# Kernel optimization log

Hardware: AMD Instinct MI355X
Metric: run time of the kernel (lower is better)

## Reference

```python
import jax, jax.numpy as jnp
import numpy as np

M, K, N = 8192, 1024, 8192

def setup_inputs() -> dict:
    key = jax.random.key(0)
    k1, k2, k3, k4 = jax.random.split(key, 4)
    # a, b are int8-valued quantized tensors (stored as int32 per harness dtype set)
    a = jax.random.randint(k1, (M, K), 0, 127, dtype=jnp.int32)
    b = jax.random.randint(k2, (K, N), 0, 127, dtype=jnp.int32)
    alpha_row = jax.random.uniform(k3, (M, 1), dtype=jnp.float32)
    alpha_col = jax.random.uniform(k4, (1, N), dtype=jnp.float32)
    return {"a": a, "b": b, "alpha_row": alpha_row, "alpha_col": alpha_col}

def reference(a, b, alpha_row, alpha_col):
    # Faithful to TorchGemmA8W8.forward: upcast int8 operands to fp32,
    # matmul with fp32 accumulate, cast result to int8.
    # (alpha_row / alpha_col are accepted but unused in this variant.)
    x = jnp.matmul(a.astype(jnp.float32), b.astype(jnp.float32))  # [M, N] fp32
    return x.astype(jnp.int8)
```

## Files before the change

### kernel.cpp

```cpp
#include <hip/hip_runtime.h>
#include <stdint.h>

#define M_DIM 8192
#define N_DIM 8192
#define K_DIM 1024
#define BK    128

typedef int int4v __attribute__((ext_vector_type(4)));

__device__ __forceinline__ void gload16(const char* g, char* l) {
    __builtin_amdgcn_global_load_lds(
        (__attribute__((address_space(1))) void*)(void*)const_cast<char*>(g),
        (__attribute__((address_space(3))) void*)l,
        16, 0, 0);
}

__device__ __forceinline__ int sat8(int v) {
    v = v > 127 ? 127 : v;
    v = v < -128 ? -128 : v;
    return v;
}

__global__ __launch_bounds__(256) void pack_ab_kernel(const int* __restrict__ a,
                                                      const int* __restrict__ b,
                                                      int* __restrict__ outA,
                                                      char* __restrict__ outB) {
    __shared__ char tile[64][68];
    const int t = threadIdx.x;
    if (blockIdx.x < 8192) {
        int i = blockIdx.x * 256 + t;
        int4 v = ((const int4*)a)[i];
        outA[i] = (v.x & 0xff) | ((v.y & 0xff) << 8) |
                  ((v.z & 0xff) << 16) | ((v.w & 0xff) << 24);
        return;
    }
    const int bx = blockIdx.x - 8192;
    const int n0 = (bx & 127) * 64;
    const int k0 = (bx >> 7) * 64;
    const int tr  = t >> 4;
    const int tc4 = (t & 15) << 2;
#pragma unroll
    for (int j = 0; j < 4; ++j) {
        int row = tr + j * 16;
        int4 v = *(const int4*)&b[(size_t)(k0 + row) * N_DIM + n0 + tc4];
        tile[row][tc4 + 0] = (char)v.x;
        tile[row][tc4 + 1] = (char)v.y;
        tile[row][tc4 + 2] = (char)v.z;
        tile[row][tc4 + 3] = (char)v.w;
    }
    __syncthreads();
#pragma unroll
    for (int j = 0; j < 4; ++j) {
        int n = tr + j * 16;
        int pk = (tile[tc4 + 0][n] & 0xff) |
                 ((tile[tc4 + 1][n] & 0xff) << 8) |
                 ((tile[tc4 + 2][n] & 0xff) << 16) |
                 ((tile[tc4 + 3][n] & 0xff) << 24);
        *(int*)&outB[(size_t)(n0 + n) * K_DIM + k0 + tc4] = pk;
    }
}

__global__ __launch_bounds__(256) void gemm_i8_kernel(const char* __restrict__ A8,
                                                      const char* __restrict__ B8,
                                                      int* __restrict__ C) {
    __shared__ __align__(16) char As[2 * 128 * 64];
    __shared__ __align__(16) char Bs[2 * 128 * 64];

    const int t    = threadIdx.x;
    const int bn   = blockIdx.x;
    const int bm   = blockIdx.y;
    const int lane = t & 63;
    const int wave = t >> 6;
    const int wm   = wave >> 1;
    const int wn   = wave & 1;
    const int quad = lane >> 4;
    const int l16  = lane & 15;

    const size_t aBase = (size_t)(bm * 128) * K_DIM;
    const size_t bBase = (size_t)(bn * 128) * K_DIM;

    const int sr = t >> 2;
    const int swzc = (((t & 3) ^ ((t >> 3) & 3)) << 4);
    const int laneByte = ((quad ^ ((l16 >> 1) & 3)) << 4);

    int4v acc[4][4] = {};

    for (int kt = 0; kt < K_DIM / BK; ++kt) {
        const int kOff = kt * BK;
#pragma unroll
        for (int s = 0; s < 4; ++s) {
            const int p = s >> 1;
            const int rr = ((s & 1) << 6) + sr;
            const int f = s * 4096 + t * 16;
            gload16(A8 + aBase + (size_t)rr * K_DIM + kOff + p * 64 + swzc, As + f);
            gload16(B8 + bBase + (size_t)rr * K_DIM + kOff + p * 64 + swzc, Bs + f);
        }
        __syncthreads();

#pragma unroll
        for (int h = 0; h < 2; ++h) {
            int4v af[4], bf[4];
#pragma unroll
            for (int mi = 0; mi < 4; ++mi)
                af[mi] = *(const int4v*)
                    &As[h * 8192 + (wm * 64 + mi * 16 + l16) * 64 + laneByte];
#pragma unroll
            for (int ni = 0; ni < 4; ++ni)
                bf[ni] = *(const int4v*)
                    &Bs[h * 8192 + (wn * 64 + ni * 16 + l16) * 64 + laneByte];

#pragma unroll
            for (int mi = 0; mi < 4; ++mi)
#pragma unroll
                for (int ni = 0; ni < 4; ++ni)
                    acc[mi][ni] = __builtin_amdgcn_mfma_i32_16x16x64_i8(
                        af[mi], bf[ni], acc[mi][ni], 0, 0, 0);
        }

        __syncthreads();
    }

    const int mBase = bm * 128 + wm * 64;
    const int nBase = bn * 128 + wn * 64;
#pragma unroll
    for (int mi = 0; mi < 4; ++mi) {
#pragma unroll
        for (int ni = 0; ni < 4; ++ni) {
            const int col = nBase + ni * 16 + l16;
#pragma unroll
            for (int r = 0; r < 4; ++r) {
                const int row = mBase + mi * 16 + quad * 4 + r;
                C[(size_t)row * N_DIM + col] = sat8(acc[mi][ni][r]);
            }
        }
    }
}

__global__ __launch_bounds__(256) void gemm_naive_kernel(const int* __restrict__ a,
                                                         const int* __restrict__ b,
                                                         int* __restrict__ C) {
    const int col = blockIdx.x * 256 + threadIdx.x;
    const int row = blockIdx.y;
    int acc = 0;
    for (int k = 0; k < K_DIM; ++k)
        acc += a[(size_t)row * K_DIM + k] * b[(size_t)k * N_DIM + col];
    C[(size_t)row * N_DIM + col] = sat8(acc);
}

extern "C" void kernel_launch(void* const* d_in, const int* in_sizes, int n_in,
                              void* d_out, int out_size, void* d_ws, size_t ws_size,
                              hipStream_t stream) {
    const int* a = (const int*)d_in[0];
    const int* b = (const int*)d_in[1];
    int* out = (int*)d_out;

    const size_t needed = 2 * (size_t)M_DIM * K_DIM;
    if (ws_size < needed) {
        gemm_naive_kernel<<<dim3(N_DIM / 256, M_DIM), 256, 0, stream>>>(a, b, out);
        return;
    }

    char* A8 = (char*)d_ws;
    char* B8 = A8 + (size_t)M_DIM * K_DIM;

    pack_ab_kernel<<<8192 + 2048, 256, 0, stream>>>(a, b, (int*)A8, B8);
    gemm_i8_kernel<<<dim3(N_DIM / 128, M_DIM / 128), 256, 0, stream>>>(A8, B8, out);
}
```

Baseline: 363.3 us.

## Triple-buffer LDS tiles with async prefetch two K-steps ahead

Replaces the load-then-sync double-half loop with a three-slot LDS ring of BK=64 tiles. Global-to-LDS loads for tile kt+2 are issued before the MFMAs of tile kt, and a single barrier per iteration is gated by s_waitcnt vmcnt(4) instead of full syncthreads. MFMA sections are wrapped in s_setprio to favour compute issue. This aims to hide global memory latency behind compute, at the cost of more LDS use, which may reduce occupancy, and redundant loads of the last tile at the tail.

```diff
diff --git a/kernel.cpp b/kernel.cpp
--- a/kernel.cpp
+++ b/kernel.cpp
@@ -4,7 +4,6 @@
 #define M_DIM 8192
 #define N_DIM 8192
 #define K_DIM 1024
-#define BK    128
 
 typedef int int4v __attribute__((ext_vector_type(4)));
 
@@ -63,8 +62,8 @@
 __global__ __launch_bounds__(256) void gemm_i8_kernel(const char* __restrict__ A8,
                                                       const char* __restrict__ B8,
                                                       int* __restrict__ C) {
-    __shared__ __align__(16) char As[2 * 128 * 64];
-    __shared__ __align__(16) char Bs[2 * 128 * 64];
+    __shared__ __align__(16) char As[3][128][64];
+    __shared__ __align__(16) char Bs[3][128][64];
 
     const int t    = threadIdx.x;
     const int bn   = blockIdx.x;
@@ -76,49 +75,62 @@
     const int quad = lane >> 4;
     const int l16  = lane & 15;
 
-    const size_t aBase = (size_t)(bm * 128) * K_DIM;
-    const size_t bBase = (size_t)(bn * 128) * K_DIM;
-
-    const int sr = t >> 2;
+    const int sr   = t >> 2;
     const int swzc = (((t & 3) ^ ((t >> 3) & 3)) << 4);
+    const char* aSrc = A8 + (size_t)(bm * 128) * K_DIM + (size_t)sr * K_DIM + swzc;
+    const char* bSrc = B8 + (size_t)(bn * 128) * K_DIM + (size_t)sr * K_DIM + swzc;
     const int laneByte = ((quad ^ ((l16 >> 1) & 3)) << 4);
+    const int aRow = wm * 64 + l16;
+    const int bRow = wn * 64 + l16;
 
     int4v acc[4][4] = {};
 
-    for (int kt = 0; kt < K_DIM / BK; ++kt) {
-        const int kOff = kt * BK;
-#pragma unroll
-        for (int s = 0; s < 4; ++s) {
-            const int p = s >> 1;
-            const int rr = ((s & 1) << 6) + sr;
-            const int f = s * 4096 + t * 16;
-            gload16(A8 + aBase + (size_t)rr * K_DIM + kOff + p * 64 + swzc, As + f);
-            gload16(B8 + bBase + (size_t)rr * K_DIM + kOff + p * 64 + swzc, Bs + f);
-        }
-        __syncthreads();
+#define STAGE(TILE, SLOT) do {                                                  \
+    const int kOff_ = (TILE) * 64;                                              \
+    gload16(aSrc + kOff_,                        &As[SLOT][0][0] + t * 16);     \
+    gload16(aSrc + (size_t)64 * K_DIM + kOff_,   &As[SLOT][0][0] + (t + 256) * 16); \
+    gload16(bSrc + kOff_,                        &Bs[SLOT][0][0] + t * 16);     \
+    gload16(bSrc + (size_t)64 * K_DIM + kOff_,   &Bs[SLOT][0][0] + (t + 256) * 16); \
+} while (0)
+
+    STAGE(0, 0);
+    STAGE(1, 1);
+    asm volatile("s_waitcnt vmcnt(4)" ::: "memory");
+    __builtin_amdgcn_s_barrier();
+    __builtin_amdgcn_sched_barrier(0);
 
 #pragma unroll
-        for (int h = 0; h < 2; ++h) {
-            int4v af[4], bf[4];
+    for (int kt = 0; kt < K_DIM / 64; ++kt) {
+        const int cur  = kt % 3;
+        const int slot = (kt + 2) % 3;
+        const int tile = (kt + 2 < K_DIM / 64) ? kt + 2 : K_DIM / 64 - 1;
+
+        int4v af[4], bf[4];
 #pragma unroll
-            for (int mi = 0; mi < 4; ++mi)
-                af[mi] = *(const int4v*)
-                    &As[h * 8192 + (wm * 64 + mi * 16 + l16) * 64 + laneByte];
+        for (int mi = 0; mi < 4; ++mi)
+            af[mi] = *(const int4v*)&As[cur][aRow + mi * 16][laneByte];
+#pragma unroll
+        for (int ni = 0; ni < 4; ++ni)
+            bf[ni] = *(const int4v*)&Bs[cur][bRow + ni * 16][laneByte];
+
+        STAGE(tile, slot);
+
+        __builtin_amdgcn_s_setprio(1);
+#pragma unroll
+        for (int mi = 0; mi < 4; ++mi)
 #pragma unroll
             for (int ni = 0; ni < 4; ++ni)
-                bf[ni] = *(const int4v*)
-                    &Bs[h * 8192 + (wn * 64 + ni * 16 + l16) * 64 + laneByte];
+                acc[mi][ni] = __builtin_amdgcn_mfma_i32_16x16x64_i8(
+                    af[mi], bf[ni], acc[mi][ni], 0, 0, 0);
+        __builtin_amdgcn_s_setprio(0);
 
-#pragma unroll
-            for (int mi = 0; mi < 4; ++mi)
-#pragma unroll
-                for (int ni = 0; ni < 4; ++ni)
-                    acc[mi][ni] = __builtin_amdgcn_mfma_i32_16x16x64_i8(
-                        af[mi], bf[ni], acc[mi][ni], 0, 0, 0);
-        }
+        asm volatile("s_waitcnt vmcnt(4)" ::: "memory");
+        __builtin_amdgcn_s_barrier();
+        __builtin_amdgcn_sched_barrier(0);
+    }
+#undef STAGE
 
-        __syncthreads();
-    }
+    asm volatile("s_waitcnt vmcnt(0)" ::: "memory");
 
     const int mBase = bm * 128 + wm * 64;
     const int nBase = bn * 128 + wn * 64;
```

Measured after the change: 372.8 us. +2.6%, slower.
